# Kernel tuning notes

Measured on AMD Instinct MI355X. Metric: run time of the kernel, lower is better.

The kernel has to match this reference:

```python
import jax, jax.numpy as jnp
import numpy as np

H = 1024
F = 4096  # base_ffn_dim = hidden * 4
WIDTHS = [256, 512]  # adapters; idx 2 -> width==hidden -> identity
EPS = 1e-5


def _xavier(key, fan_in, fan_out, gain):
    a = gain * np.sqrt(6.0 / (fan_in + fan_out))
    return jax.random.uniform(key, (fan_in, fan_out), jnp.float32, -a, a)


def _layernorm(x, g, b):
    mu = jnp.mean(x, axis=-1, keepdims=True)
    var = jnp.var(x, axis=-1, keepdims=True)
    return (x - mu) * jax.lax.rsqrt(var + EPS) * g + b


def setup_inputs() -> dict:
    key = jax.random.key(0)
    ks = jax.random.split(key, 12)
    g = 1.0 / np.sqrt(2.0)
    B, S = 4, 2048
    return {
        "x": jax.random.normal(ks[0], (B, S, H), jnp.float32),
        "width_multiplier": jax.random.uniform(ks[1], (B, S, 1), jnp.float32),
        "width_idx": jax.random.randint(ks[2], (B, S), 0, 3, jnp.int32),
        "ln_in_g": jnp.ones((H,), jnp.float32),
        "ln_in_b": jnp.zeros((H,), jnp.float32),
        "W1": _xavier(ks[3], H, F, g),
        "b1": jnp.zeros((F,), jnp.float32),
        "ln_h_g": jnp.ones((F,), jnp.float32),
        "ln_h_b": jnp.zeros((F,), jnp.float32),
        "W2": _xavier(ks[4], F, H, g),
        "b2": jnp.zeros((H,), jnp.float32),
        "a256_w1": _xavier(ks[5], H, 256, g),
        "a256_b1": jnp.zeros((256,), jnp.float32),
        "a256_w2": _xavier(ks[6], 256, H, g),
        "a256_b2": jnp.zeros((H,), jnp.float32),
        "a512_w1": _xavier(ks[7], H, 512, g),
        "a512_b1": jnp.zeros((512,), jnp.float32),
        "a512_w2": _xavier(ks[8], 512, H, g),
        "a512_b2": jnp.zeros((H,), jnp.float32),
    }


def reference(x, width_multiplier, width_idx,
              ln_in_g, ln_in_b, W1, b1, ln_h_g, ln_h_b, W2, b2,
              a256_w1, a256_b1, a256_w2, a256_b2,
              a512_w1, a512_b1, a512_w2, a512_b2):
    gelu = lambda t: jax.nn.gelu(t, approximate=False)  # torch nn.GELU exact
    x_norm = _layernorm(x, ln_in_g, ln_in_b)
    # base FFN path
    h = gelu(jnp.einsum("bsh,hf->bsf", x_norm, W1) + b1)
    h = _layernorm(h, ln_h_g, ln_h_b)
    base = jnp.einsum("bsf,fh->bsh", h, W2) + b2
    # width adapters (routed per token by width_idx)
    ad0 = jnp.einsum("bsw,wh->bsh", gelu(jnp.einsum("bsh,hw->bsw", x_norm, a256_w1) + a256_b1), a256_w2) + a256_b2
    ad1 = jnp.einsum("bsw,wh->bsh", gelu(jnp.einsum("bsh,hw->bsw", x_norm, a512_w1) + a512_b1), a512_w2) + a512_b2
    idx = width_idx[..., None]
    adaptive = jnp.where(idx == 0, ad0, jnp.where(idx == 1, ad1, x_norm))
    return base * width_multiplier + adaptive * (1.0 - width_multiplier)
```

## Files before the change

### kernel.cpp

```cpp
#include <hip/hip_runtime.h>
#include <cstdint>
#include <cstddef>

typedef unsigned short u16x8 __attribute__((ext_vector_type(8)));
typedef unsigned short u16x4 __attribute__((ext_vector_type(4)));
typedef __bf16 bf16x8 __attribute__((ext_vector_type(8)));
typedef float f32x4 __attribute__((ext_vector_type(4)));

__device__ __forceinline__ float b2f(unsigned short u) {
    union { unsigned int i; float f; } v;
    v.i = ((unsigned int)u) << 16;
    return v.f;
}

__device__ __forceinline__ unsigned short f2b(float f) {
    union { float f; unsigned int i; } v;
    v.f = f;
    unsigned int x = v.i;
    unsigned int lsb = (x >> 16) & 1u;
    x += 0x7FFFu + lsb;
    return (unsigned short)(x >> 16);
}

__device__ __forceinline__ float gelu_exact(float x) {
    return 0.5f * x * (1.0f + erff(x * 0.70710678118654752f));
}

__device__ __forceinline__ void ld_lds16(const unsigned short* g, unsigned short* l) {
    __builtin_amdgcn_global_load_lds(
        (const __attribute__((address_space(1))) void*)g,
        (__attribute__((address_space(3))) void*)l, 16, 0, 0);
}


__device__ __forceinline__ void transp_body(const float* __restrict__ in,
                                            unsigned short* __restrict__ out,
                                            int R, int C, int ldout,
                                            const float* __restrict__ scale,
                                            int bx, int by) {
    __shared__ float tile[32][33];
    const int tx = threadIdx.x & 31;
    const int ty = threadIdx.x >> 5;
    int x = bx * 32 + tx;
    int y0 = by * 32;
    for (int k = 0; k < 32; k += 8)
        tile[ty + k][tx] = in[(size_t)(y0 + ty + k) * C + x];
    __syncthreads();
    int ox = y0 + tx;
    int oy = bx * 32;
    float sc = scale ? scale[ox] : 1.0f;
    for (int k = 0; k < 32; k += 8)
        out[(size_t)(oy + ty + k) * ldout + ox] = f2b(tile[tx][ty + k] * sc);
}

__device__ __forceinline__ void c01_partial_body(const float* __restrict__ W2,
                                                 const float* __restrict__ g,
                                                 const float* __restrict__ b,
                                                 float* __restrict__ pc0,
                                                 float* __restrict__ pc1,
                                                 int N, int kc, int nb) {
    int n = (nb << 8) + threadIdx.x;
    int k0 = kc << 8;
    float p0 = 0.f, p1 = 0.f;
    for (int k = k0; k < k0 + 256; ++k) {
        float w = W2[(size_t)k * N + n];
        p0 += b[k] * w;
        p1 += g[k] * w;
    }
    pc0[kc * 1024 + n] = p0;
    pc1[kc * 1024 + n] = p1;
}

__device__ __forceinline__ void ln1024_body(const float* __restrict__ in,
                                            unsigned short* __restrict__ out,
                                            const float* __restrict__ g,
                                            const float* __restrict__ b,
                                            int row) {
    const int t = threadIdx.x;
    f32x4 v = ((const f32x4*)(in + (size_t)row * 1024))[t];
    float s = v[0] + v[1] + v[2] + v[3];
    float s2 = v[0] * v[0] + v[1] * v[1] + v[2] * v[2] + v[3] * v[3];
#pragma unroll
    for (int o = 32; o > 0; o >>= 1) {
        s  += __shfl_down(s, o, 64);
        s2 += __shfl_down(s2, o, 64);
    }
    __shared__ float red[8];
    int lane = t & 63, w = t >> 6;
    if (lane == 0) { red[w] = s; red[4 + w] = s2; }
    __syncthreads();
    if (t == 0) {
        red[0] = red[0] + red[1] + red[2] + red[3];
        red[4] = red[4] + red[5] + red[6] + red[7];
    }
    __syncthreads();
    const float inv_n = 1.0f / 1024.0f;
    float mu = red[0] * inv_n;
    float var = red[4] * inv_n - mu * mu;
    float rs = rsqrtf(var + 1e-5f);
    f32x4 gv = ((const f32x4*)g)[t];
    f32x4 bv = ((const f32x4*)b)[t];
    u16x4 ov;
#pragma unroll
    for (int r = 0; r < 4; ++r) ov[r] = f2b((v[r] - mu) * rs * gv[r] + bv[r]);
    ((u16x4*)(out + (size_t)row * 1024))[t] = ov;
}

__device__ __forceinline__ void rowstats_body(const unsigned short* __restrict__ h,
                                              float* __restrict__ st, int row) {
    const int t = threadIdx.x;
    const u16x8* p = (const u16x8*)(h + (size_t)row * 4096);
    float s = 0.f, s2 = 0.f;
#pragma unroll
    for (int i = 0; i < 2; ++i) {
        u16x8 v = p[t + (i << 8)];
#pragma unroll
        for (int r = 0; r < 8; ++r) { float f = b2f(v[r]); s += f; s2 += f * f; }
    }
#pragma unroll
    for (int o = 32; o > 0; o >>= 1) {
        s  += __shfl_down(s, o, 64);
        s2 += __shfl_down(s2, o, 64);
    }
    __shared__ float red2[8];
    int lane = t & 63, w = t >> 6;
    if (lane == 0) { red2[w] = s; red2[4 + w] = s2; }
    __syncthreads();
    if (t == 0) {
        float ss = red2[0] + red2[1] + red2[2] + red2[3];
        float qq = red2[4] + red2[5] + red2[6] + red2[7];
        const float inv = 1.0f / 4096.0f;
        float mu = ss * inv;
        float var = qq * inv - mu * mu;
        float rs = rsqrtf(var + 1e-5f);
        st[2 * (size_t)row]     = rs;
        st[2 * (size_t)row + 1] = rs * mu;
    }
}

template <int EPI>
__device__ __forceinline__ void gemm_body(
    unsigned short (*As)[128 * 32], unsigned short (*Bs)[128 * 32],
    int fid, int nbx, int nby,
    const unsigned short* __restrict__ A, int lda,
    const unsigned short* __restrict__ BT, int ldb,
    const float* __restrict__ bias, unsigned short* __restrict__ Cb,
    float* __restrict__ Cf, int N, int K,
    const int* __restrict__ idx,
    const float* __restrict__ wm,
    const unsigned short* __restrict__ adaptive,
    const unsigned short* __restrict__ xn,
    const float* __restrict__ c1v,
    const float* __restrict__ rstat) {
    const int t = threadIdx.x;

    int id = fid;
    const int nwg = nbx * nby;
    if ((nwg & 7) == 0) {
        const int cpx = nwg >> 3;
        id = (id & 7) * cpx + (id >> 3);
    }
    const int bx = id % nbx;
    const int by = id / nbx;
    const int m0 = by * 128;
    const int n0 = bx * 128;

    const int lane = t & 63;
    const int wid = t >> 6;

    const int srow = lane >> 2;
    const int sch  = (lane & 3) ^ (srow & 3);
    const int scol = sch << 3;

    const int wr = (wid >> 1) << 6;
    const int wc = (wid & 1) << 6;
    const int ml = lane & 15;
    const int q = lane >> 4;
    const int qsw = ((q ^ (ml & 3)) << 3);

    f32x4 acc[4][4];
#pragma unroll
    for (int i = 0; i < 4; ++i)
#pragma unroll
        for (int j = 0; j < 4; ++j)
#pragma unroll
            for (int r = 0; r < 4; ++r) acc[i][j][r] = 0.0f;

    const int nk = K >> 5;

#define STAGE(KT, BUF)                                                          \
    {                                                                           \
        _Pragma("unroll")                                                       \
        for (int hh = 0; hh < 2; ++hh) {                                        \
            int rbase = wid * 32 + hh * 16;                                     \
            int row = rbase + srow;                                             \
            ld_lds16(A  + (size_t)(m0 + row) * lda + (KT) * 32 + scol,          \
                     &As[BUF][rbase * 32]);                                     \
            ld_lds16(BT + (size_t)(n0 + row) * ldb + (KT) * 32 + scol,          \
                     &Bs[BUF][rbase * 32]);                                     \
        }                                                                       \
    }

    STAGE(0, 0);
    for (int kt = 0; kt < nk; ++kt) {
        const int cur = kt & 1;
        __syncthreads();
        if (kt + 1 < nk) STAGE(kt + 1, cur ^ 1);

        bf16x8 af[4], bf[4];
#pragma unroll
        for (int i = 0; i < 4; ++i)
            af[i] = *(const bf16x8*)(&As[cur][(wr + i * 16 + ml) * 32 + qsw]);
#pragma unroll
        for (int j = 0; j < 4; ++j)
            bf[j] = *(const bf16x8*)(&Bs[cur][(wc + j * 16 + ml) * 32 + qsw]);
#pragma unroll
        for (int i = 0; i < 4; ++i)
#pragma unroll
            for (int j = 0; j < 4; ++j)
                acc[i][j] = __builtin_amdgcn_mfma_f32_16x16x32_bf16(af[i], bf[j], acc[i][j], 0, 0, 0);
    }
#undef STAGE

#pragma unroll
    for (int i = 0; i < 4; ++i) {
        float rsv[4], rmv[4], wv[4];
        int idv[4];
        if (EPI != 0) {
#pragma unroll
            for (int r = 0; r < 4; ++r) {
                int row = m0 + wr + i * 16 + q * 4 + r;
                idv[r] = idx[row];
                if (EPI == 2) {
                    wv[r] = wm[row];
                    rsv[r] = rstat[2 * (size_t)row];
                    rmv[r] = rstat[2 * (size_t)row + 1];
                }
            }
        }
#pragma unroll
        for (int j = 0; j < 4; ++j) {
            int col = n0 + wc + j * 16 + ml;
            float bv = bias[col];
            float bv1 = (EPI == 4) ? bias[1024 + col] : 0.0f;
            float c1c = (EPI == 2) ? c1v[col] : 0.0f;
#pragma unroll
            for (int r = 0; r < 4; ++r) {
                int row = m0 + wr + i * 16 + q * 4 + r;
                size_t off = (size_t)row * N + col;
                if (EPI == 0) {
                    Cb[off] = f2b(gelu_exact(acc[i][j][r] + bv));
                } else if (EPI == 3) {
                    bool act = (col < 256) ? (idv[r] == 0) : (idv[r] == 1);
                    Cb[off] = f2b(act ? gelu_exact(acc[i][j][r] + bv) : 0.0f);
                } else if (EPI == 4) {
                    float bsel = (idv[r] == 1) ? bv1 : bv;
                    Cb[off] = f2b(acc[i][j][r] + bsel);
                } else {
                    float bval = rsv[r] * acc[i][j][r] + bv - rmv[r] * c1c;
                    float a = b2f((idv[r] <= 1) ? adaptive[off] : xn[off]);
                    Cf[off] = bval * wv[r] + a * (1.0f - wv[r]);
                }
            }
        }
    }
}

__global__ __launch_bounds__(256) void mega_prep(
    const float* __restrict__ W1, const float* __restrict__ W2,
    const float* __restrict__ ln_h_g, const float* __restrict__ ln_h_b,
    const float* __restrict__ a256_w1, const float* __restrict__ a512_w1,
    const float* __restrict__ a256_w2, const float* __restrict__ a512_w2,
    const float* __restrict__ a256_b1, const float* __restrict__ a512_b1,
    const float* __restrict__ a256_b2, const float* __restrict__ a512_b2,
    const float* __restrict__ x, const float* __restrict__ ln_in_g,
    const float* __restrict__ ln_in_b,
    unsigned short* __restrict__ W1T, unsigned short* __restrict__ W2T,
    unsigned short* __restrict__ awup, unsigned short* __restrict__ awdT,
    float* __restrict__ ab1, float* __restrict__ b2sel,
    float* __restrict__ pc0, float* __restrict__ pc1,
    unsigned short* __restrict__ xn) {
    const int H = 1024, F = 4096;
    int bid = blockIdx.x;
    if (bid < 4096) {
        transp_body(W1, W1T, H, F, H, nullptr, bid & 127, bid >> 7);
    } else if (bid < 8192) {
        int l = bid - 4096;
        transp_body(W2, W2T, F, H, F, ln_h_g, l & 31, l >> 5);
    } else if (bid < 8448) {
        int l = bid - 8192;
        transp_body(a256_w1, awup, H, 256, H, nullptr, l & 7, l >> 3);
    } else if (bid < 8960) {
        int l = bid - 8448;
        transp_body(a512_w1, awup + (size_t)256 * H, H, 512, H, nullptr, l & 15, l >> 4);
    } else if (bid < 9216) {
        int l = bid - 8960;
        transp_body(a256_w2, awdT, 256, H, 768, nullptr, l & 31, l >> 5);
    } else if (bid < 9728) {
        int l = bid - 9216;
        transp_body(a512_w2, awdT + 256, 512, H, 768, nullptr, l & 31, l >> 5);
    } else if (bid < 9731) {
        int n = (bid - 9728) * 256 + threadIdx.x;
        if (n < 768) ab1[n] = (n < 256) ? a256_b1[n] : a512_b1[n - 256];
    } else if (bid < 9739) {
        int n = (bid - 9731) * 256 + threadIdx.x;
        b2sel[n] = (n < 1024) ? a256_b2[n] : a512_b2[n - 1024];
    } else if (bid < 9803) {
        int l = bid - 9739;
        c01_partial_body(W2, ln_h_g, ln_h_b, pc0, pc1, H, l >> 2, l & 3);
    } else {
        ln1024_body(x, xn, ln_in_g, ln_in_b, bid - 9803);
    }
}

__global__ __launch_bounds__(256) void gemm1(
    const unsigned short* __restrict__ xn, const unsigned short* __restrict__ W1T,
    const float* __restrict__ b1, unsigned short* __restrict__ h) {
    __shared__ __align__(16) unsigned short As[2][128 * 32];
    __shared__ __align__(16) unsigned short Bs[2][128 * 32];
    gemm_body<0>(As, Bs, blockIdx.y * gridDim.x + blockIdx.x,
                 gridDim.x, gridDim.y, xn, 1024, W1T, 1024, b1, h,
                 nullptr, 4096, 1024, nullptr, nullptr, nullptr, nullptr,
                 nullptr, nullptr);
}

__global__ __launch_bounds__(256) void up_stats(
    const unsigned short* __restrict__ xn, const unsigned short* __restrict__ awup,
    const float* __restrict__ ab1, unsigned short* __restrict__ tt,
    const int* __restrict__ widx,
    const unsigned short* __restrict__ h, float* __restrict__ st) {
    __shared__ __align__(16) unsigned short As[2][128 * 32];
    __shared__ __align__(16) unsigned short Bs[2][128 * 32];
    int bid = blockIdx.x;
    if (bid < 384) {
        gemm_body<3>(As, Bs, bid, 6, 64, xn, 1024, awup, 1024, ab1, tt,
                     nullptr, 768, 1024, widx, nullptr, nullptr, nullptr,
                     nullptr, nullptr);
    } else {
        rowstats_body(h, st, bid - 384);
    }
}

__global__ __launch_bounds__(256) void mid_k(
    const unsigned short* __restrict__ tt, const unsigned short* __restrict__ awdT,
    const float* __restrict__ b2sel, unsigned short* __restrict__ adp,
    const int* __restrict__ widx,
    const float* __restrict__ pc0, const float* __restrict__ pc1,
    const float* __restrict__ b2, float* __restrict__ c0b2,
    float* __restrict__ c1) {
    __shared__ __align__(16) unsigned short As[2][128 * 32];
    __shared__ __align__(16) unsigned short Bs[2][128 * 32];
    int bid = blockIdx.x;
    if (bid < 512) {
        gemm_body<4>(As, Bs, bid, 8, 64, tt, 768, awdT, 768, b2sel, adp,
                     nullptr, 1024, 768, widx, nullptr, nullptr, nullptr,
                     nullptr, nullptr);
    } else {
        int n = ((bid - 512) << 8) + threadIdx.x;
        float s0 = b2[n], s1 = 0.f;
#pragma unroll
        for (int kc = 0; kc < 16; ++kc) {
            s0 += pc0[kc * 1024 + n];
            s1 += pc1[kc * 1024 + n];
        }
        c0b2[n] = s0;
        c1[n] = s1;
    }
}

__global__ __launch_bounds__(256) void gemm_fin(
    const unsigned short* __restrict__ A, int lda,
    const unsigned short* __restrict__ BT, int ldb,
    const float* __restrict__ bias, float* __restrict__ Cf, int N, int K,
    const int* __restrict__ idx, const float* __restrict__ wm,
    const unsigned short* __restrict__ adaptive,
    const unsigned short* __restrict__ xn,
    const float* __restrict__ c1v, const float* __restrict__ rstat) {
    __shared__ __align__(16) unsigned short As[2][128 * 32];
    __shared__ __align__(16) unsigned short Bs[2][128 * 32];
    gemm_body<2>(As, Bs, blockIdx.y * gridDim.x + blockIdx.x,
                 gridDim.x, gridDim.y, A, lda, BT, ldb, bias, nullptr, Cf, N, K,
                 idx, wm, adaptive, xn, c1v, rstat);
}

extern "C" void kernel_launch(void* const* d_in, const int* in_sizes, int n_in,
                              void* d_out, int out_size, void* d_ws, size_t ws_size,
                              hipStream_t stream) {
    const float* x       = (const float*)d_in[0];
    const float* wm      = (const float*)d_in[1];
    const int*   widx    = (const int*)d_in[2];
    const float* ln_in_g = (const float*)d_in[3];
    const float* ln_in_b = (const float*)d_in[4];
    const float* W1      = (const float*)d_in[5];
    const float* b1      = (const float*)d_in[6];
    const float* ln_h_g  = (const float*)d_in[7];
    const float* ln_h_b  = (const float*)d_in[8];
    const float* W2      = (const float*)d_in[9];
    const float* b2      = (const float*)d_in[10];
    const float* a256_w1 = (const float*)d_in[11];
    const float* a256_b1 = (const float*)d_in[12];
    const float* a256_w2 = (const float*)d_in[13];
    const float* a256_b2 = (const float*)d_in[14];
    const float* a512_w1 = (const float*)d_in[15];
    const float* a512_b1 = (const float*)d_in[16];
    const float* a512_w2 = (const float*)d_in[17];
    const float* a512_b2 = (const float*)d_in[18];
    float* out = (float*)d_out;

    const int T = 8192, H = 1024, F = 4096;

    unsigned short* ws0   = (unsigned short*)d_ws;
    unsigned short* xn    = ws0;
    unsigned short* h     = xn    + (size_t)T * H;
    unsigned short* tt    = h     + (size_t)T * F;
    unsigned short* adp   = tt    + (size_t)T * 768;
    unsigned short* W1T   = adp   + (size_t)T * H;
    unsigned short* W2T   = W1T   + (size_t)H * F;
    unsigned short* awup  = W2T   + (size_t)F * H;
    unsigned short* awdT  = awup  + (size_t)768 * H;
    float*          ab1   = (float*)(awdT + (size_t)H * 768);
    float*          b2sel = ab1 + 768;
    float*          stats = b2sel + 2048;
    float*          c0b2  = stats + (size_t)T * 2;
    float*          c1    = c0b2 + H;
    float*          pc0   = c1 + H;
    float*          pc1   = pc0 + 16 * 1024;

    mega_prep<<<9803 + T, 256, 0, stream>>>(
        W1, W2, ln_h_g, ln_h_b, a256_w1, a512_w1, a256_w2, a512_w2,
        a256_b1, a512_b1, a256_b2, a512_b2, x, ln_in_g, ln_in_b,
        W1T, W2T, awup, awdT, ab1, b2sel, pc0, pc1, xn);

    gemm1<<<dim3(F / 128, T / 128), 256, 0, stream>>>(xn, W1T, b1, h);

    up_stats<<<384 + T, 256, 0, stream>>>(xn, awup, ab1, tt, widx, h, stats);

    mid_k<<<512 + 4, 256, 0, stream>>>(tt, awdT, b2sel, adp, widx,
                                       pc0, pc1, b2, c0b2, c1);

    gemm_fin<<<dim3(H / 128, T / 128), 256, 0, stream>>>(
        h, F, W2T, F, c0b2, out, H, F, widx, wm, adp, xn, c1, stats);
}
```

Measured before the change: 414.8 us.

## Merge adapter up-GEMM into gemm1 launch and move row stats into mid kernel

Fuses the base up-projection GEMM and the adapter up-projection GEMM into a single launch, and moves the hidden-row statistics pass into the adapter down-projection kernel. This removes one kernel launch and its boundary, and lets the small adapter GEMM fill the tail wave of the large GEMM. The cost is that row stats now share a launch with the down-projection GEMM, and the block-index mapping for gemm1 changes from a 2D grid to a 1D index.

```diff
diff --git a/kernel.cpp b/kernel.cpp
--- a/kernel.cpp
+++ b/kernel.cpp
@@ -313,31 +313,22 @@
     }
 }
 
-__global__ __launch_bounds__(256) void gemm1(
+__global__ __launch_bounds__(256) void big(
     const unsigned short* __restrict__ xn, const unsigned short* __restrict__ W1T,
-    const float* __restrict__ b1, unsigned short* __restrict__ h) {
-    __shared__ __align__(16) unsigned short As[2][128 * 32];
-    __shared__ __align__(16) unsigned short Bs[2][128 * 32];
-    gemm_body<0>(As, Bs, blockIdx.y * gridDim.x + blockIdx.x,
-                 gridDim.x, gridDim.y, xn, 1024, W1T, 1024, b1, h,
-                 nullptr, 4096, 1024, nullptr, nullptr, nullptr, nullptr,
-                 nullptr, nullptr);
-}
-
-__global__ __launch_bounds__(256) void up_stats(
-    const unsigned short* __restrict__ xn, const unsigned short* __restrict__ awup,
-    const float* __restrict__ ab1, unsigned short* __restrict__ tt,
-    const int* __restrict__ widx,
-    const unsigned short* __restrict__ h, float* __restrict__ st) {
+    const float* __restrict__ b1, unsigned short* __restrict__ h,
+    const unsigned short* __restrict__ awup, const float* __restrict__ ab1,
+    unsigned short* __restrict__ tt, const int* __restrict__ widx) {
     __shared__ __align__(16) unsigned short As[2][128 * 32];
     __shared__ __align__(16) unsigned short Bs[2][128 * 32];
     int bid = blockIdx.x;
-    if (bid < 384) {
-        gemm_body<3>(As, Bs, bid, 6, 64, xn, 1024, awup, 1024, ab1, tt,
+    if (bid < 2048) {
+        gemm_body<0>(As, Bs, bid, 32, 64, xn, 1024, W1T, 1024, b1, h,
+                     nullptr, 4096, 1024, nullptr, nullptr, nullptr, nullptr,
+                     nullptr, nullptr);
+    } else {
+        gemm_body<3>(As, Bs, bid - 2048, 6, 64, xn, 1024, awup, 1024, ab1, tt,
                      nullptr, 768, 1024, widx, nullptr, nullptr, nullptr,
                      nullptr, nullptr);
-    } else {
-        rowstats_body(h, st, bid - 384);
     }
 }
 
@@ -345,6 +336,7 @@
     const unsigned short* __restrict__ tt, const unsigned short* __restrict__ awdT,
     const float* __restrict__ b2sel, unsigned short* __restrict__ adp,
     const int* __restrict__ widx,
+    const unsigned short* __restrict__ h, float* __restrict__ stats,
     const float* __restrict__ pc0, const float* __restrict__ pc1,
     const float* __restrict__ b2, float* __restrict__ c0b2,
     float* __restrict__ c1) {
@@ -355,8 +347,10 @@
         gemm_body<4>(As, Bs, bid, 8, 64, tt, 768, awdT, 768, b2sel, adp,
                      nullptr, 1024, 768, widx, nullptr, nullptr, nullptr,
                      nullptr, nullptr);
+    } else if (bid < 8704) {
+        rowstats_body(h, stats, bid - 512);
     } else {
-        int n = ((bid - 512) << 8) + threadIdx.x;
+        int n = ((bid - 8704) << 8) + threadIdx.x;
         float s0 = b2[n], s1 = 0.f;
 #pragma unroll
         for (int kc = 0; kc < 16; ++kc) {
@@ -431,12 +425,10 @@
         a256_b1, a512_b1, a256_b2, a512_b2, x, ln_in_g, ln_in_b,
         W1T, W2T, awup, awdT, ab1, b2sel, pc0, pc1, xn);
 
-    gemm1<<<dim3(F / 128, T / 128), 256, 0, stream>>>(xn, W1T, b1, h);
-
-    up_stats<<<384 + T, 256, 0, stream>>>(xn, awup, ab1, tt, widx, h, stats);
-
-    mid_k<<<512 + 4, 256, 0, stream>>>(tt, awdT, b2sel, adp, widx,
-                                       pc0, pc1, b2, c0b2, c1);
+    big<<<2048 + 384, 256, 0, stream>>>(xn, W1T, b1, h, awup, ab1, tt, widx);
+
+    mid_k<<<512 + 8192 + 4, 256, 0, stream>>>(
+        tt, awdT, b2sel, adp, widx, h, stats, pc0, pc1, b2, c0b2, c1);
 
     gemm_fin<<<dim3(H / 128, T / 128), 256, 0, stream>>>(
         h, F, W2T, F, c0b2, out, H, F, widx, wm, adp, xn, c1, stats);
```

Measured after the change: 436.1 us. 1.05x slower.
